# Kernel optimization log

Measured on AMD Instinct MI355X. Metric: run time of the kernel, lower is better.

Reference implementation:

```python
import jax, jax.numpy as jnp
import numpy as np

B, N, H, HEADS = 4, 4096, 256, 8
DEG = 16
E = B * N * DEG  # 262144 edges
DH = H // HEADS


def setup_inputs() -> dict:
    key = jax.random.key(0)
    ks = jax.random.split(key, 8)
    node_states = jax.random.normal(ks[0], (B, N, H), dtype=jnp.float32)
    # edge_indices rows: [batch_idx, target_node, source_node]
    b_idx = jnp.repeat(jnp.arange(B, dtype=jnp.int64), N * DEG)
    tgt = jnp.tile(jnp.repeat(jnp.arange(N, dtype=jnp.int64), DEG), B)
    src = jax.random.randint(ks[1], (E,), 0, N, dtype=jnp.int64)
    edge_indices = jnp.stack([b_idx, tgt, src])  # (3, E)
    s = 1.0 / np.sqrt(H)
    Wq = jax.random.normal(ks[2], (H, H), dtype=jnp.float32) * s
    Wk = jax.random.normal(ks[3], (H, H), dtype=jnp.float32) * s
    Wv = jax.random.normal(ks[4], (H, H), dtype=jnp.float32) * s
    bq = jnp.zeros((H,), dtype=jnp.float32)
    bk = jnp.zeros((H,), dtype=jnp.float32)
    bv = jnp.zeros((H,), dtype=jnp.float32)
    return {"node_states": node_states, "edge_indices": edge_indices,
            "Wq": Wq, "bq": bq, "Wk": Wk, "bk": bk, "Wv": Wv, "bv": bv}


def reference(node_states, edge_indices, Wq, bq, Wk, bk, Wv, bv):
    batch, n_nodes, hidden = node_states.shape
    b_idx, tgt, src = edge_indices[0], edge_indices[1], edge_indices[2]
    num_edges = b_idx.shape[0]

    # Dense Q/K/V projections on nodes (cheap), then per-edge gathers.
    Q = (node_states @ Wq + bq).reshape(batch, n_nodes, HEADS, DH)
    K = (node_states @ Wk + bk).reshape(batch, n_nodes, HEADS, DH)
    V = (node_states @ Wv + bv).reshape(batch, n_nodes, HEADS, DH)

    q_e = Q[b_idx, tgt]  # (E, heads, dh)
    k_e = K[b_idx, src]  # (E, heads, dh)
    scores = jnp.sum(q_e * k_e, axis=-1) / jnp.sqrt(jnp.float32(DH))  # (E, heads)

    # Segment softmax over source nodes, grouped per (batch, target) --
    # mirrors torch.sparse.softmax(logits, dim=-2).
    seg = b_idx * n_nodes + tgt  # (E,)
    num_seg = batch * n_nodes
    m = jax.ops.segment_max(scores, seg, num_segments=num_seg)  # (B*N, heads)
    exp = jnp.exp(scores - m[seg])
    denom = jax.ops.segment_sum(exp, seg, num_segments=num_seg)
    attn = exp / denom[seg]  # (E, heads)

    # Weighted scatter-sum of source values into target nodes
    # (replaces sparse edge_mask @ elwise_prod).
    v_e = V[b_idx, src]  # (E, heads, dh)
    weighted = (attn[..., None] * v_e).reshape(num_edges, hidden)
    out = jax.ops.segment_sum(weighted, seg, num_segments=num_seg)
    return out.reshape(batch, n_nodes, hidden)
```

## Files before the change

kernel.cpp:

```cpp
#include <hip/hip_runtime.h>
#include <hip/hip_bf16.h>

#define BATCH 4
#define NNODES 4096
#define HID 256
#define NHEADS 8
#define DH 32
#define DEG 16
#define NEDGES (BATCH * NNODES * DEG)
#define NROWS (BATCH * NNODES)

typedef __attribute__((ext_vector_type(8))) short short8;
typedef __attribute__((ext_vector_type(8))) unsigned short ushort8;
typedef __attribute__((ext_vector_type(4))) unsigned short u16x4;
typedef __attribute__((ext_vector_type(4))) float f32x4;

static __device__ __forceinline__ unsigned short f2bf(float f) {
  __hip_bfloat16 h = __float2bfloat16(f);
  return *reinterpret_cast<unsigned short*>(&h);
}
static __device__ __forceinline__ float bf2f(unsigned short u) {
  unsigned int v = ((unsigned int)u) << 16;
  return *reinterpret_cast<float*>(&v);
}

#define XBLOCKS 2048
#define WBLOCKS 96
__global__ __launch_bounds__(256) void prep_kernel(
    const float* __restrict__ X,
    const float* __restrict__ Wq, const float* __restrict__ Wk,
    const float* __restrict__ Wv,
    unsigned short* __restrict__ Xb, unsigned short* __restrict__ Wt) {
  const int tid = threadIdx.x;
  if (blockIdx.x < XBLOCKS) {
    const size_t base = (size_t)blockIdx.x * 2048 + (size_t)tid * 8;
    const float4 a = *reinterpret_cast<const float4*>(&X[base]);
    const float4 b = *reinterpret_cast<const float4*>(&X[base + 4]);
    ushort8 o;
    o[0] = f2bf(a.x); o[1] = f2bf(a.y); o[2] = f2bf(a.z); o[3] = f2bf(a.w);
    o[4] = f2bf(b.x); o[5] = f2bf(b.y); o[6] = f2bf(b.z); o[7] = f2bf(b.w);
    *reinterpret_cast<ushort8*>(&Xb[base]) = o;
  } else {
    const int o = (blockIdx.x - XBLOCKS) * 2048 + tid * 8;
    const int mat   = o >> 16;
    const int w     = o & 65535;
    const int strip = w >> 14;
    const int r     = w & 16383;
    const int kk    = r >> 11;
    const int hi    = (r >> 9) & 3;
    const int col   = (r >> 3) & 63;
    const int k0    = kk * 32 + hi * 8;
    const int c     = strip * 64 + col;
    const float* __restrict__ W = (mat == 0) ? Wq : (mat == 1) ? Wk : Wv;
    ushort8 ovec;
    #pragma unroll
    for (int j = 0; j < 8; ++j) {
      ovec[j] = f2bf(W[(size_t)(k0 + j) * HID + c]);
    }
    *reinterpret_cast<ushort8*>(&Wt[o]) = ovec;
  }
}

__global__ __launch_bounds__(256, 6) void qkv_mfma_kernel(
    const unsigned short* __restrict__ Xb, const unsigned short* __restrict__ Wt,
    const float* __restrict__ bq, const float* __restrict__ bk,
    const float* __restrict__ bv,
    float* __restrict__ Qs, unsigned short* __restrict__ Kb,
    unsigned short* __restrict__ Vb) {
  const int tid = threadIdx.x;
  const int xcd = blockIdx.x & 7;
  const int l = blockIdx.x >> 3;
  const int s = l % 12;
  const int chunk = (l / 12) * 8 + xcd;
  const int mat = s >> 2;
  const int cs = s & 3;
  const int c0 = cs * 64;

  const int lane = tid & 63;
  const int wv = tid >> 6;
  const int lm = lane & 15;
  const int hi = lane >> 4;
  const int lk = hi * 8;
  const int row = chunk * 64 + wv * 16 + lm;

  short8 Af[8];
  #pragma unroll
  for (int kk = 0; kk < 8; ++kk) {
    Af[kk] = *reinterpret_cast<const short8*>(
        &Xb[(size_t)row * 256 + kk * 32 + lk]);
  }

  const unsigned short* __restrict__ Wm = Wt + (size_t)(mat * 4 + cs) * 16384;
  const float* __restrict__ bias = (mat == 0) ? bq : (mat == 1) ? bk : bv;

  #pragma unroll
  for (int nt = 0; nt < 4; ++nt) {
    short8 Bf[8];
    #pragma unroll
    for (int kk = 0; kk < 8; ++kk) {
      Bf[kk] = *reinterpret_cast<const short8*>(
          &Wm[kk * 2048 + hi * 512 + (nt * 16 + lm) * 8]);
    }
    f32x4 acc = {0.f, 0.f, 0.f, 0.f};
    #pragma unroll
    for (int kk = 0; kk < 8; ++kk) {
      acc = __builtin_amdgcn_mfma_f32_16x16x32_bf16(Bf[kk], Af[kk], acc, 0, 0, 0);
    }
    const int col0 = c0 + nt * 16 + hi * 4;
    const float4 b4 = *reinterpret_cast<const float4*>(&bias[col0]);
    if (mat == 0) {
      float4 o;
      o.x = acc[0] + b4.x; o.y = acc[1] + b4.y;
      o.z = acc[2] + b4.z; o.w = acc[3] + b4.w;
      *reinterpret_cast<float4*>(&Qs[(size_t)row * 256 + col0]) = o;
    } else {
      u16x4 o;
      o[0] = f2bf(acc[0] + b4.x); o[1] = f2bf(acc[1] + b4.y);
      o[2] = f2bf(acc[2] + b4.z); o[3] = f2bf(acc[3] + b4.w);
      unsigned short* __restrict__ dst = (mat == 1) ? Kb : Vb;
      *reinterpret_cast<u16x4*>(&dst[(size_t)row * 256 + col0]) = o;
    }
  }
}

__global__ __launch_bounds__(256) void attn_kernel(
    const float* __restrict__ Q, const unsigned short* __restrict__ K,
    const unsigned short* __restrict__ V, const int* __restrict__ edges,
    float* __restrict__ out) {
  __shared__ float s_w[DEG * NHEADS];

  const int bx = blockIdx.x;
  const int xcd = bx & 7;
  const int g = (xcd >> 1) * NNODES + (((bx >> 3) << 1) | (xcd & 1));
  const int e0 = g * DEG;
  const int tid = threadIdx.x;

  const int b = edges[e0];
  const int qrow = b * NNODES + edges[NEDGES + e0];

  const int lane = tid & 63;
  const int wv = tid >> 6;
  const int j = lane >> 2;
  const int hh = (lane >> 1) & 1;
  const int p = lane & 1;
  const int h = wv * 2 + hh;
  const int ch0 = h * 32 + p * 16;

  const int nsrc = b * NNODES + edges[2 * NEDGES + e0 + j];

  const float* __restrict__ qp = &Q[(size_t)qrow * HID + ch0];
  const float4 q0 = *reinterpret_cast<const float4*>(qp);
  const float4 q1 = *reinterpret_cast<const float4*>(qp + 4);
  const float4 q2 = *reinterpret_cast<const float4*>(qp + 8);
  const float4 q3 = *reinterpret_cast<const float4*>(qp + 12);
  const unsigned short* __restrict__ kp = &K[(size_t)nsrc * HID + ch0];
  const ushort8 k0 = *reinterpret_cast<const ushort8*>(kp);
  const ushort8 k1 = *reinterpret_cast<const ushort8*>(kp + 8);

  float partial;
  partial  = q0.x * bf2f(k0[0]); partial = fmaf(q0.y, bf2f(k0[1]), partial);
  partial = fmaf(q0.z, bf2f(k0[2]), partial); partial = fmaf(q0.w, bf2f(k0[3]), partial);
  partial = fmaf(q1.x, bf2f(k0[4]), partial); partial = fmaf(q1.y, bf2f(k0[5]), partial);
  partial = fmaf(q1.z, bf2f(k0[6]), partial); partial = fmaf(q1.w, bf2f(k0[7]), partial);
  partial = fmaf(q2.x, bf2f(k1[0]), partial); partial = fmaf(q2.y, bf2f(k1[1]), partial);
  partial = fmaf(q2.z, bf2f(k1[2]), partial); partial = fmaf(q2.w, bf2f(k1[3]), partial);
  partial = fmaf(q3.x, bf2f(k1[4]), partial); partial = fmaf(q3.y, bf2f(k1[5]), partial);
  partial = fmaf(q3.z, bf2f(k1[6]), partial); partial = fmaf(q3.w, bf2f(k1[7]), partial);

  partial += __shfl_xor(partial, 1);
  const float sc = partial * 0.17677669529663687f;

  const float e = __expf(sc);
  float sum = e;
  sum += __shfl_xor(sum, 4);
  sum += __shfl_xor(sum, 8);
  sum += __shfl_xor(sum, 16);
  sum += __shfl_xor(sum, 32);

  if (p == 0) s_w[j * NHEADS + h] = e / sum;
  asm volatile("s_waitcnt lgkmcnt(0)" ::: "memory");

  const int h3 = tid >> 5;
  float acc = 0.0f;
  #pragma unroll
  for (int jj = 0; jj < DEG; ++jj) {
    const int n = b * NNODES + edges[2 * NEDGES + e0 + jj];
    acc = fmaf(s_w[jj * NHEADS + h3], bf2f(V[(size_t)n * HID + tid]), acc);
  }
  out[(size_t)qrow * HID + tid] = acc;
}

extern "C" void kernel_launch(void* const* d_in, const int* in_sizes, int n_in,
                              void* d_out, int out_size, void* d_ws, size_t ws_size,
                              hipStream_t stream) {
  const float* X     = (const float*)d_in[0];
  const int*   edges = (const int*)d_in[1];
  const float* Wq    = (const float*)d_in[2];
  const float* bq    = (const float*)d_in[3];
  const float* Wk    = (const float*)d_in[4];
  const float* bk    = (const float*)d_in[5];
  const float* Wv    = (const float*)d_in[6];
  const float* bv    = (const float*)d_in[7];
  float* out = (float*)d_out;

  char* w = (char*)d_ws;
  float*          Qs = (float*)w;                 w += (size_t)NROWS * HID * 4;
  unsigned short* Kb = (unsigned short*)w;        w += (size_t)NROWS * HID * 2;
  unsigned short* Vb = (unsigned short*)w;        w += (size_t)NROWS * HID * 2;
  unsigned short* Xb = (unsigned short*)w;        w += (size_t)NROWS * HID * 2;
  unsigned short* Wt = (unsigned short*)w;

  prep_kernel<<<XBLOCKS + WBLOCKS, 256, 0, stream>>>(X, Wq, Wk, Wv, Xb, Wt);
  qkv_mfma_kernel<<<3072, 256, 0, stream>>>(Xb, Wt, bq, bk, bv, Qs, Kb, Vb);
  attn_kernel<<<NROWS, 256, 0, stream>>>(Qs, Kb, Vb, edges, out);
}
```

Before: 68.67 us.

## Stage weight strip in LDS and loop QKV blocks over four row chunks

Result: slower. 71.15 us (+3.6%).

```diff
diff --git a/kernel.cpp b/kernel.cpp
--- a/kernel.cpp
+++ b/kernel.cpp
@@ -61,64 +61,102 @@
   }
 }
 
-__global__ __launch_bounds__(256, 6) void qkv_mfma_kernel(
+__global__ __launch_bounds__(256, 3) void qkv_mfma_kernel(
     const unsigned short* __restrict__ Xb, const unsigned short* __restrict__ Wt,
     const float* __restrict__ bq, const float* __restrict__ bk,
     const float* __restrict__ bv,
     float* __restrict__ Qs, unsigned short* __restrict__ Kb,
     unsigned short* __restrict__ Vb) {
+  __shared__ unsigned short sW[16384];
+
   const int tid = threadIdx.x;
   const int xcd = blockIdx.x & 7;
-  const int l = blockIdx.x >> 3;
-  const int s = l % 12;
-  const int chunk = (l / 12) * 8 + xcd;
+  const int ll = blockIdx.x >> 3;
+  const int s = ll % 12;
+  const int sub = ll / 12;
   const int mat = s >> 2;
   const int cs = s & 3;
   const int c0 = cs * 64;
+  const int chunk0 = sub * 32 + xcd * 4;
+
+  const unsigned short* __restrict__ Wsrc = Wt + (size_t)(mat * 4 + cs) * 16384;
+  #pragma unroll
+  for (int i = 0; i < 8; ++i) {
+    const int e = i * 2048 + tid * 8;
+    *reinterpret_cast<ushort8*>(&sW[e]) =
+        *reinterpret_cast<const ushort8*>(&Wsrc[e]);
+  }
 
   const int lane = tid & 63;
   const int wv = tid >> 6;
   const int lm = lane & 15;
   const int hi = lane >> 4;
   const int lk = hi * 8;
-  const int row = chunk * 64 + wv * 16 + lm;
-
-  short8 Af[8];
-  #pragma unroll
-  for (int kk = 0; kk < 8; ++kk) {
-    Af[kk] = *reinterpret_cast<const short8*>(
-        &Xb[(size_t)row * 256 + kk * 32 + lk]);
-  }
-
-  const unsigned short* __restrict__ Wm = Wt + (size_t)(mat * 4 + cs) * 16384;
+  const int rbase = wv * 16 + lm;
+
   const float* __restrict__ bias = (mat == 0) ? bq : (mat == 1) ? bk : bv;
-
+  float4 b4v[4];
   #pragma unroll
   for (int nt = 0; nt < 4; ++nt) {
-    short8 Bf[8];
+    b4v[nt] = *reinterpret_cast<const float4*>(&bias[c0 + nt * 16 + hi * 4]);
+  }
+
+  short8 Aa[8], Ab[8];
+  {
+    const int row = chunk0 * 64 + rbase;
     #pragma unroll
     for (int kk = 0; kk < 8; ++kk) {
-      Bf[kk] = *reinterpret_cast<const short8*>(
-          &Wm[kk * 2048 + hi * 512 + (nt * 16 + lm) * 8]);
-    }
-    f32x4 acc = {0.f, 0.f, 0.f, 0.f};
+      Aa[kk] = *reinterpret_cast<const short8*>(
+          &Xb[(size_t)row * 256 + kk * 32 + lk]);
+    }
+  }
+  __syncthreads();
+
+  #pragma unroll
+  for (int it = 0; it < 4; ++it) {
+    if (it < 3) {
+      const int rown = (chunk0 + it + 1) * 64 + rbase;
+      #pragma unroll
+      for (int kk = 0; kk < 8; ++kk) {
+        if (it & 1) {
+          Aa[kk] = *reinterpret_cast<const short8*>(
+              &Xb[(size_t)rown * 256 + kk * 32 + lk]);
+        } else {
+          Ab[kk] = *reinterpret_cast<const short8*>(
+              &Xb[(size_t)rown * 256 + kk * 32 + lk]);
+        }
+      }
+    }
+    const int row = (chunk0 + it) * 64 + rbase;
+
     #pragma unroll
-    for (int kk = 0; kk < 8; ++kk) {
-      acc = __builtin_amdgcn_mfma_f32_16x16x32_bf16(Bf[kk], Af[kk], acc, 0, 0, 0);
-    }
-    const int col0 = c0 + nt * 16 + hi * 4;
-    const float4 b4 = *reinterpret_cast<const float4*>(&bias[col0]);
-    if (mat == 0) {
-      float4 o;
-      o.x = acc[0] + b4.x; o.y = acc[1] + b4.y;
-      o.z = acc[2] + b4.z; o.w = acc[3] + b4.w;
-      *reinterpret_cast<float4*>(&Qs[(size_t)row * 256 + col0]) = o;
-    } else {
-      u16x4 o;
-      o[0] = f2bf(acc[0] + b4.x); o[1] = f2bf(acc[1] + b4.y);
-      o[2] = f2bf(acc[2] + b4.z); o[3] = f2bf(acc[3] + b4.w);
-      unsigned short* __restrict__ dst = (mat == 1) ? Kb : Vb;
-      *reinterpret_cast<u16x4*>(&dst[(size_t)row * 256 + col0]) = o;
+    for (int nt = 0; nt < 4; ++nt) {
+      short8 Bf[8];
+      #pragma unroll
+      for (int kk = 0; kk < 8; ++kk) {
+        Bf[kk] = *reinterpret_cast<const short8*>(
+            &sW[kk * 2048 + hi * 512 + (nt * 16 + lm) * 8]);
+      }
+      f32x4 acc = {0.f, 0.f, 0.f, 0.f};
+      #pragma unroll
+      for (int kk = 0; kk < 8; ++kk) {
+        acc = __builtin_amdgcn_mfma_f32_16x16x32_bf16(
+            Bf[kk], (it & 1) ? Ab[kk] : Aa[kk], acc, 0, 0, 0);
+      }
+      const int col0 = c0 + nt * 16 + hi * 4;
+      const float4 b4 = b4v[nt];
+      if (mat == 0) {
+        float4 o;
+        o.x = acc[0] + b4.x; o.y = acc[1] + b4.y;
+        o.z = acc[2] + b4.z; o.w = acc[3] + b4.w;
+        *reinterpret_cast<float4*>(&Qs[(size_t)row * 256 + col0]) = o;
+      } else {
+        u16x4 o;
+        o[0] = f2bf(acc[0] + b4.x); o[1] = f2bf(acc[1] + b4.y);
+        o[2] = f2bf(acc[2] + b4.z); o[3] = f2bf(acc[3] + b4.w);
+        unsigned short* __restrict__ dst = (mat == 1) ? Kb : Vb;
+        *reinterpret_cast<u16x4*>(&dst[(size_t)row * 256 + col0]) = o;
+      }
     }
   }
 }
@@ -211,6 +249,6 @@
   unsigned short* Wt = (unsigned short*)w;
 
   prep_kernel<<<XBLOCKS + WBLOCKS, 256, 0, stream>>>(X, Wq, Wk, Wv, Xb, Wt);
-  qkv_mfma_kernel<<<3072, 256, 0, stream>>>(Xb, Wt, bq, bk, bv, Qs, Kb, Vb);
+  qkv_mfma_kernel<<<768, 256, 0, stream>>>(Xb, Wt, bq, bk, bv, Qs, Kb, Vb);
   attn_kernel<<<NROWS, 256, 0, stream>>>(Qs, Kb, Vb, edges, out);
 }
```

## Stage weight tile in LDS for QKV GEMM and prefetch V rows early in attention

Applied to the files above, without the earlier changes.

Measured after the change: 62.38 us. 9.2% less time.

```diff
diff --git a/kernel.cpp b/kernel.cpp
--- a/kernel.cpp
+++ b/kernel.cpp
@@ -61,20 +61,27 @@
   }
 }
 
-__global__ __launch_bounds__(256, 6) void qkv_mfma_kernel(
+__global__ __launch_bounds__(256, 4) void qkv_mfma_kernel(
     const unsigned short* __restrict__ Xb, const unsigned short* __restrict__ Wt,
     const float* __restrict__ bq, const float* __restrict__ bk,
     const float* __restrict__ bv,
     float* __restrict__ Qs, unsigned short* __restrict__ Kb,
     unsigned short* __restrict__ Vb) {
+  __shared__ unsigned short sW[16384];
+
   const int tid = threadIdx.x;
-  const int xcd = blockIdx.x & 7;
-  const int l = blockIdx.x >> 3;
-  const int s = l % 12;
-  const int chunk = (l / 12) * 8 + xcd;
+  const int s = blockIdx.x >> 8;
+  const int chunk = blockIdx.x & 255;
   const int mat = s >> 2;
-  const int cs = s & 3;
-  const int c0 = cs * 64;
+  const int c0 = (s & 3) * 64;
+
+  const unsigned short* __restrict__ Wsrc = Wt + (size_t)(mat * 4 + (s & 3)) * 16384;
+  #pragma unroll
+  for (int i = 0; i < 8; ++i) {
+    const int e = i * 2048 + tid * 8;
+    *reinterpret_cast<ushort8*>(&sW[e]) =
+        *reinterpret_cast<const ushort8*>(&Wsrc[e]);
+  }
 
   const int lane = tid & 63;
   const int wv = tid >> 6;
@@ -90,8 +97,9 @@
         &Xb[(size_t)row * 256 + kk * 32 + lk]);
   }
 
-  const unsigned short* __restrict__ Wm = Wt + (size_t)(mat * 4 + cs) * 16384;
   const float* __restrict__ bias = (mat == 0) ? bq : (mat == 1) ? bk : bv;
+
+  __syncthreads();
 
   #pragma unroll
   for (int nt = 0; nt < 4; ++nt) {
@@ -99,7 +107,7 @@
     #pragma unroll
     for (int kk = 0; kk < 8; ++kk) {
       Bf[kk] = *reinterpret_cast<const short8*>(
-          &Wm[kk * 2048 + hi * 512 + (nt * 16 + lm) * 8]);
+          &sW[kk * 2048 + hi * 512 + (nt * 16 + lm) * 8]);
     }
     f32x4 acc = {0.f, 0.f, 0.f, 0.f};
     #pragma unroll
@@ -136,7 +144,15 @@
   const int tid = threadIdx.x;
 
   const int b = edges[e0];
-  const int qrow = b * NNODES + edges[NEDGES + e0];
+  const int bN = b * NNODES;
+  const int qrow = bN + edges[NEDGES + e0];
+
+  unsigned short vraw[DEG];
+  #pragma unroll
+  for (int jj = 0; jj < DEG; ++jj) {
+    const int n = bN + edges[2 * NEDGES + e0 + jj];
+    vraw[jj] = V[(size_t)n * HID + tid];
+  }
 
   const int lane = tid & 63;
   const int wv = tid >> 6;
@@ -146,7 +162,7 @@
   const int h = wv * 2 + hh;
   const int ch0 = h * 32 + p * 16;
 
-  const int nsrc = b * NNODES + edges[2 * NEDGES + e0 + j];
+  const int nsrc = bN + edges[2 * NEDGES + e0 + j];
 
   const float* __restrict__ qp = &Q[(size_t)qrow * HID + ch0];
   const float4 q0 = *reinterpret_cast<const float4*>(qp);
@@ -184,8 +200,7 @@
   float acc = 0.0f;
   #pragma unroll
   for (int jj = 0; jj < DEG; ++jj) {
-    const int n = b * NNODES + edges[2 * NEDGES + e0 + jj];
-    acc = fmaf(s_w[jj * NHEADS + h3], bf2f(V[(size_t)n * HID + tid]), acc);
+    acc = fmaf(s_w[jj * NHEADS + h3], bf2f(vraw[jj]), acc);
   }
   out[(size_t)qrow * HID + tid] = acc;
 }
```
